# Kernel optimization log

Hardware: AMD Instinct MI355X
Metric: run time of the kernel (lower is better)

Reference implementation:

```python
import jax, jax.numpy as jnp
import numpy as np

N_NODES = 20000
N_EDGES = 200000
N_GRAPHS = 128
IN_DIM = 256
HID = 512
HEADS = 8
C = HID // HEADS  # 64
LAT = 256
NEG_SLOPE = 0.2
BN_EPS = 1e-5


def setup_inputs() -> dict:
    key = jax.random.key(0)
    ks = jax.random.split(key, 24)
    n = lambda k, s, sc=0.05: jax.random.normal(k, s, jnp.float32) * sc
    return {
        'x': jax.random.normal(ks[0], (N_NODES, IN_DIM), jnp.float32),
        'edge_index': jax.random.randint(ks[1], (2, N_EDGES), 0, N_NODES, jnp.int32),
        'batch': jnp.sort(jax.random.randint(ks[2], (N_NODES,), 0, N_GRAPHS, jnp.int32)),
        'Wl0': n(ks[3], (IN_DIM, HID)), 'bl0': n(ks[4], (HID,)),
        'Wr0': n(ks[5], (IN_DIM, HID)), 'br0': n(ks[6], (HID,)),
        'att0': n(ks[7], (HEADS, C)), 'bias0': n(ks[8], (HID,)),
        'Wl1': n(ks[9], (HID, HID)), 'bl1': n(ks[10], (HID,)),
        'Wr1': n(ks[11], (HID, HID)), 'br1': n(ks[12], (HID,)),
        'att1': n(ks[13], (HEADS, C)), 'bias1': n(ks[14], (HID,)),
        'bn_gamma': jnp.ones((HID,), jnp.float32),
        'bn_beta': jnp.zeros((HID,), jnp.float32),
        'bn_mean': n(ks[15], (HID,)),
        'bn_var': jax.random.uniform(ks[16], (HID,), jnp.float32, 0.5, 1.5),
        'Wfc': n(ks[17], (HID, LAT)), 'bfc': n(ks[18], (LAT,)),
    }


def gatv2_layer(x, src, dst, Wl, bl, Wr, br, att, bias):
    # x: [N, F]; returns [N, HEADS*C]. GATv2: e = a . LeakyReLU(Wl x_src + Wr x_dst)
    xl = (x @ Wl + bl).reshape(-1, HEADS, C)  # source transform [N,H,C]
    xr = (x @ Wr + br).reshape(-1, HEADS, C)  # target transform [N,H,C]
    feat = jax.nn.leaky_relu(xl[src] + xr[dst], NEG_SLOPE)     # [E,H,C]
    logits = jnp.einsum('ehc,hc->eh', feat, att)               # [E,H]
    # segment softmax over incoming edges of each target node
    m = jax.ops.segment_max(logits, dst, num_segments=N_NODES)  # [N,H]
    p = jnp.exp(logits - m[dst])
    denom = jax.ops.segment_sum(p, dst, num_segments=N_NODES)   # [N,H]
    alpha = p / (denom[dst] + 1e-16)                            # [E,H]
    msg = xl[src] * alpha[:, :, None]                           # [E,H,C]
    out = jax.ops.segment_sum(msg, dst, num_segments=N_NODES)   # [N,H,C]
    return out.reshape(-1, HEADS * C) + bias


def reference(x, edge_index, batch, Wl0, bl0, Wr0, br0, att0, bias0,
              Wl1, bl1, Wr1, br1, att1, bias1,
              bn_gamma, bn_beta, bn_mean, bn_var, Wfc, bfc):
    src, dst = edge_index[0], edge_index[1]
    # layer 0 + ELU (dropout is identity in eval mode)
    h = jax.nn.elu(gatv2_layer(x, src, dst, Wl0, bl0, Wr0, br0, att0, bias0))
    # layer 1 + ELU
    h = jax.nn.elu(gatv2_layer(h, src, dst, Wl1, bl1, Wr1, br1, att1, bias1))
    # global add pool over graphs
    g = jax.ops.segment_sum(h, batch, num_segments=N_GRAPHS)  # [G, HID]
    # BatchNorm1d (eval mode: running stats)
    g = (g - bn_mean) * jax.lax.rsqrt(bn_var + BN_EPS) * bn_gamma + bn_beta
    return g @ Wfc + bfc  # [G, LAT]
```

## Files before the change

kernel.cpp:

```cpp
#include <hip/hip_runtime.h>
#include <hip/hip_bf16.h>
#include <cstdint>

#define NN 20000
#define NE 200000
#define NG 128
#define HID 512
#define XLR_W 1024

typedef __attribute__((ext_vector_type(4))) float f32x4;
typedef __attribute__((ext_vector_type(8))) short s16x8;

__device__ __forceinline__ float bf2f(unsigned short u) {
  union { unsigned int i; float f; } v; v.i = ((unsigned int)u) << 16; return v.f;
}
__device__ __forceinline__ unsigned short f2bf(float f) {
  union { float f; unsigned int i; } v; v.f = f;
  unsigned int i = v.i + 0x7FFFu + ((v.i >> 16) & 1u);
  return (unsigned short)(i >> 16);
}
__device__ __forceinline__ float asf(unsigned int u) {
  union { unsigned int i; float f; } v; v.i = u; return v.f;
}

#define GLOAD16(gp, lp)                                                        \
  __builtin_amdgcn_global_load_lds(                                            \
      (const __attribute__((address_space(1))) unsigned int*)(gp),             \
      (__attribute__((address_space(3))) unsigned int*)(lp), 16, 0, 0)

__global__ __launch_bounds__(256) void k_prep(const float* __restrict__ x,
                                              unsigned short* __restrict__ xb,
                                              const float* __restrict__ Wl0, const float* __restrict__ bl0,
                                              const float* __restrict__ Wr0, const float* __restrict__ br0,
                                              unsigned short* __restrict__ wt0, float* __restrict__ bcat0,
                                              const float* __restrict__ Wl1, const float* __restrict__ bl1,
                                              const float* __restrict__ Wr1, const float* __restrict__ br1,
                                              unsigned short* __restrict__ wt1, float* __restrict__ bcat1,
                                              int* __restrict__ deg) {
  int b = blockIdx.x, t = threadIdx.x;
  if (b < 79) {
    int i = b * 256 + t;
    if (i < NN) deg[i] = 0;
  } else if (b < 5079) {
    int i = (b - 79) * 256 + t;
    float4 v = ((const float4*)x)[i];
    ushort4 o;
    o.x = f2bf(v.x); o.y = f2bf(v.y); o.z = f2bf(v.z); o.w = f2bf(v.w);
    ((ushort4*)xb)[i] = o;
  } else if (b < 6103) {
    int id = (b - 5079) * 256 + t;
    int nrow = id >> 8, k = id & 255;
    float v = (nrow < HID) ? Wl0[k * HID + nrow] : Wr0[k * HID + (nrow - HID)];
    wt0[id] = f2bf(v);
    if (id < XLR_W) bcat0[id] = (id < HID) ? bl0[id] : br0[id - HID];
  } else {
    int id = (b - 6103) * 256 + t;
    int nrow = id >> 9, k = id & 511;
    float v = (nrow < HID) ? Wl1[k * HID + nrow] : Wr1[k * HID + (nrow - HID)];
    wt1[id] = f2bf(v);
    if (id < XLR_W) bcat1[id] = (id < HID) ? bl1[id] : br1[id - HID];
  }
}

__global__ void k_hist(const int* __restrict__ dst, int* __restrict__ deg, int E) {
  int i = blockIdx.x * blockDim.x + threadIdx.x;
  if (i < E) atomicAdd(&deg[dst[i]], 1);
}

__global__ __launch_bounds__(1024) void k_scan1(const int* __restrict__ deg,
                                                int* __restrict__ offs,
                                                int* __restrict__ btot, int n) {
  __shared__ int wsum[16];
  int t = threadIdx.x;
  int wid = t >> 6, lane = t & 63;
  int i = blockIdx.x * 1024 + t;
  int v = (i < n) ? deg[i] : 0;
  int s = v;
#pragma unroll
  for (int off = 1; off < 64; off <<= 1) {
    int x = __shfl_up(s, off, 64);
    if (lane >= off) s += x;
  }
  if (lane == 63) wsum[wid] = s;
  __syncthreads();
  if (wid == 0) {
    int ws = (lane < 16) ? wsum[lane] : 0;
#pragma unroll
    for (int off = 1; off < 16; off <<= 1) {
      int x = __shfl_up(ws, off, 64);
      if (lane >= off) ws += x;
    }
    if (lane < 16) wsum[lane] = ws;
  }
  __syncthreads();
  int ex = s - v + (wid ? wsum[wid - 1] : 0);
  if (i < n) offs[i] = ex;
  if (t == 1023) btot[blockIdx.x] = ex + v;
}

__global__ __launch_bounds__(1024) void k_scan3(int* __restrict__ offs,
                                                const int* __restrict__ btot,
                                                int* __restrict__ woff, int n, int nb) {
  __shared__ int sbofs;
  int t = threadIdx.x;
  if (t < 64) {
    int v = (t < nb) ? btot[t] : 0;
    int s = v;
#pragma unroll
    for (int off = 1; off < 64; off <<= 1) {
      int x = __shfl_up(s, off, 64);
      if (t >= off) s += x;
    }
    if (t == (int)blockIdx.x) sbofs = s - v;
    if (blockIdx.x == (unsigned)(nb - 1) && t == nb - 1) offs[n] = s;
  }
  __syncthreads();
  int add = sbofs;
  int i = blockIdx.x * 1024 + t;
  if (i < n) {
    int v = offs[i] + add;
    offs[i] = v;
    woff[i] = v;
  }
}

__global__ void k_scatter(const int* __restrict__ src, const int* __restrict__ dst,
                          int* __restrict__ woff, int* __restrict__ src_s, int E) {
  int i = blockIdx.x * blockDim.x + threadIdx.x;
  if (i < E) {
    int d = dst[i];
    int pos = atomicAdd(&woff[d], 1);
    src_s[pos] = src[i];
  }
}

#define BM 128
#define BN 128
#define PLN 4096

__global__ __launch_bounds__(256) void k_gemm(const unsigned short* __restrict__ A,
                                              const unsigned short* __restrict__ Bt,
                                              const float* __restrict__ bias,
                                              unsigned short* __restrict__ C,
                                              int M, int N, int K, int nby) {
  int L = blockIdx.x;
  int by = (L & 7) | ((L >> 6) << 3);
  int bx = (L >> 3) & 7;
  if (by >= nby) return;
  int m0 = by * BM, n0 = bx * BN;

  __shared__ __align__(16) unsigned short As[2 * PLN];
  __shared__ __align__(16) unsigned short Bs[2 * PLN];
  int t = threadIdx.x;
  int wave = t >> 6, lane = t & 63;
  int wm = (wave >> 1) * 64, wn = (wave & 1) * 64;
  int ml = lane & 15, mq = lane >> 4;
  int lr = lane >> 2;
  int qg = (lane & 3) ^ ((lane >> 3) & 3);
  int lq = qg * 8;

  f32x4 acc[4][4];
#pragma unroll
  for (int i = 0; i < 4; i++)
#pragma unroll
    for (int j = 0; j < 4; j++) acc[i][j] = (f32x4)0.0f;

  const unsigned short* gA[4];
  const unsigned short* gB[4];
  unsigned short* lA[4];
  unsigned short* lB[4];
#pragma unroll
  for (int p = 0; p < 2; p++)
#pragma unroll
    for (int h = 0; h < 2; h++) {
      int idx = p * 2 + h;
      int arow = m0 + wave * 32 + h * 16 + lr; if (arow > M - 1) arow = M - 1;
      gA[idx] = A + (size_t)arow * K + p * 32 + lq;
      gB[idx] = Bt + (size_t)(n0 + wave * 32 + h * 16 + lr) * K + p * 32 + lq;
      lA[idx] = &As[p * PLN + (wave * 32 + h * 16) * 32];
      lB[idx] = &Bs[p * PLN + (wave * 32 + h * 16) * 32];
    }

  int qr = (mq ^ ((ml >> 1) & 3)) * 8;

  int T = K >> 6;
  for (int tt = 0; tt < T; tt++) {
#pragma unroll
    for (int idx = 0; idx < 4; idx++) {
      GLOAD16(gA[idx], lA[idx]);
      GLOAD16(gB[idx], lB[idx]);
      gA[idx] += 64; gB[idx] += 64;
    }
    __syncthreads();
#pragma unroll
    for (int kq = 0; kq < 2; kq++) {
      s16x8 af[4], bfr[4];
#pragma unroll
      for (int i = 0; i < 4; i++)
        af[i] = *(const s16x8*)(&As[kq * PLN + (wm + i * 16 + ml) * 32 + qr]);
#pragma unroll
      for (int j = 0; j < 4; j++)
        bfr[j] = *(const s16x8*)(&Bs[kq * PLN + (wn + j * 16 + ml) * 32 + qr]);
#pragma unroll
      for (int i = 0; i < 4; i++)
#pragma unroll
        for (int j = 0; j < 4; j++)
          acc[i][j] = __builtin_amdgcn_mfma_f32_16x16x32_bf16(af[i], bfr[j], acc[i][j], 0, 0, 0);
    }
    __syncthreads();
  }

#pragma unroll
  for (int i = 0; i < 4; i++) {
#pragma unroll
    for (int j = 0; j < 4; j++) {
      int col = n0 + wn + j * 16 + ml;
      float bcol = bias[col];
#pragma unroll
      for (int r = 0; r < 4; r++) {
        int row = m0 + wm + i * 16 + mq * 4 + r;
        if (row < M) C[(size_t)row * N + col] = f2bf(acc[i][j][r] + bcol);
      }
    }
  }
}

__global__ __launch_bounds__(256) void k_attn(const unsigned short* __restrict__ xlr,
                                              const float* __restrict__ att,
                                              const int* __restrict__ offs,
                                              const int* __restrict__ src_s,
                                              const float* __restrict__ bias,
                                              unsigned short* __restrict__ hout) {
  __shared__ float red[4][8][68];
  __shared__ float reds[4][8];
  int n = blockIdx.x;
  int wave = threadIdx.x >> 6, lane = threadIdx.x & 63;
  int h = lane >> 3, k = lane & 7;
  int c = h * 64 + k * 8;
  int s0 = offs[n], s1 = offs[n + 1];

  uint4 uxr = *(const uint4*)(xlr + (size_t)n * XLR_W + HID + c);
  float xr[8];
  xr[0] = asf(uxr.x << 16); xr[1] = asf(uxr.x & 0xFFFF0000u);
  xr[2] = asf(uxr.y << 16); xr[3] = asf(uxr.y & 0xFFFF0000u);
  xr[4] = asf(uxr.z << 16); xr[5] = asf(uxr.z & 0xFFFF0000u);
  xr[6] = asf(uxr.w << 16); xr[7] = asf(uxr.w & 0xFFFF0000u);
  float at[8];
  {
    const float4* ap = (const float4*)(att + c);
    float4 a0 = ap[0], a1 = ap[1];
    at[0] = a0.x; at[1] = a0.y; at[2] = a0.z; at[3] = a0.w;
    at[4] = a1.x; at[5] = a1.y; at[6] = a1.z; at[7] = a1.w;
  }

  float acc[8] = {0.f, 0.f, 0.f, 0.f, 0.f, 0.f, 0.f, 0.f};
  float sum = 0.0f;

  int i = s0 + wave;
  uint4 u_cur = make_uint4(0, 0, 0, 0);
  if (i < s1) {
    int s = src_s[i];
    u_cur = *(const uint4*)(xlr + (size_t)s * XLR_W + c);
  }
  int nx = i + 4;
  for (; i < s1; i += 4) {
    uint4 u = u_cur;
    if (nx < s1) {
      int s = src_s[nx];
      u_cur = *(const uint4*)(xlr + (size_t)s * XLR_W + c);
    }
    nx += 4;

    float xl[8];
    xl[0] = asf(u.x << 16); xl[1] = asf(u.x & 0xFFFF0000u);
    xl[2] = asf(u.y << 16); xl[3] = asf(u.y & 0xFFFF0000u);
    xl[4] = asf(u.z << 16); xl[5] = asf(u.z & 0xFFFF0000u);
    xl[6] = asf(u.w << 16); xl[7] = asf(u.w & 0xFFFF0000u);

    float l = 0.0f;
#pragma unroll
    for (int j = 0; j < 8; j++) {
      float v = xl[j] + xr[j];
      v = fmaf(0.4f, fabsf(v), 0.6f * v);
      l = fmaf(v, at[j], l);
    }
    l += __shfl_xor(l, 1, 64);
    l += __shfl_xor(l, 2, 64);
    l += __shfl_xor(l, 4, 64);

    float p = __expf(l);
    sum += p;
#pragma unroll
    for (int j = 0; j < 8; j++) acc[j] = fmaf(p, xl[j], acc[j]);
  }

#pragma unroll
  for (int j = 0; j < 8; j++) red[wave][h][k * 8 + j] = acc[j];
  if (k == 0) reds[wave][h] = sum;
  __syncthreads();

  int t = threadIdx.x;
  int cc = t * 2;
  int hh = cc >> 6, off = cc & 63;
  float a0 = red[0][hh][off] + red[1][hh][off] + red[2][hh][off] + red[3][hh][off];
  float a1 = red[0][hh][off + 1] + red[1][hh][off + 1] + red[2][hh][off + 1] + red[3][hh][off + 1];
  float sm = reds[0][hh] + reds[1][hh] + reds[2][hh] + reds[3][hh];
  float di = 1.0f / (sm + 1e-16f);
  float o_a = a0 * di + bias[cc];
  float o_b = a1 * di + bias[cc + 1];
  o_a = o_a > 0.0f ? o_a : (__expf(o_a) - 1.0f);
  o_b = o_b > 0.0f ? o_b : (__expf(o_b) - 1.0f);
  unsigned int up = (unsigned int)f2bf(o_a) | ((unsigned int)f2bf(o_b) << 16);
  *(unsigned int*)(hout + (size_t)n * HID + cc) = up;
}

__device__ __forceinline__ int lower_bound(const int* __restrict__ a, int n, int key) {
  int lo = 0, hi = n;
  while (lo < hi) { int mid = (lo + hi) >> 1; if (a[mid] < key) lo = mid + 1; else hi = mid; }
  return lo;
}

__global__ __launch_bounds__(256) void k_pool(const unsigned short* __restrict__ h,
                                              const int* __restrict__ batch,
                                              float* __restrict__ part) {
  int g = blockIdx.x, p = blockIdx.y, t = threadIdx.x;
  int start = lower_bound(batch, NN, g);
  int end = lower_bound(batch, NN, g + 1);
  int cntq = (end - start + 3) >> 2;
  int lo = start + p * cntq;
  int hi = lo + cntq; if (hi > end) hi = end;
  int c = t * 2;
  float a0 = 0.0f, a1 = 0.0f;
  for (int n = lo; n < hi; n++) {
    unsigned int u = *(const unsigned int*)(h + (size_t)n * HID + c);
    a0 += asf(u << 16);
    a1 += asf(u & 0xFFFF0000u);
  }
  float* dstp = part + ((size_t)g * 4 + p) * HID + c;
  dstp[0] = a0;
  dstp[1] = a1;
}

__global__ __launch_bounds__(256) void k_fc(const float* __restrict__ part,
                                            const float* __restrict__ gamma,
                                            const float* __restrict__ beta,
                                            const float* __restrict__ mean,
                                            const float* __restrict__ var,
                                            const float* __restrict__ Wfc,
                                            const float* __restrict__ bfc,
                                            float* __restrict__ out) {
  __shared__ float xsm[512];
  int g = blockIdx.x, t = threadIdx.x;
  for (int c = t; c < HID; c += 256) {
    float s = part[((size_t)g * 4 + 0) * HID + c] + part[((size_t)g * 4 + 1) * HID + c]
            + part[((size_t)g * 4 + 2) * HID + c] + part[((size_t)g * 4 + 3) * HID + c];
    xsm[c] = (s - mean[c]) * rsqrtf(var[c] + 1e-5f) * gamma[c] + beta[c];
  }
  __syncthreads();
  float acc = bfc[t];
#pragma unroll 8
  for (int k = 0; k < 512; k++) acc += xsm[k] * Wfc[k * 256 + t];
  out[g * 256 + t] = acc;
}

extern "C" void kernel_launch(void* const* d_in, const int* in_sizes, int n_in,
                              void* d_out, int out_size, void* d_ws, size_t ws_size,
                              hipStream_t stream) {
  const float* x     = (const float*)d_in[0];
  const int* ei      = (const int*)d_in[1];
  const int* batch   = (const int*)d_in[2];
  const float* Wl0   = (const float*)d_in[3];
  const float* bl0   = (const float*)d_in[4];
  const float* Wr0   = (const float*)d_in[5];
  const float* br0   = (const float*)d_in[6];
  const float* att0  = (const float*)d_in[7];
  const float* bias0 = (const float*)d_in[8];
  const float* Wl1   = (const float*)d_in[9];
  const float* bl1   = (const float*)d_in[10];
  const float* Wr1   = (const float*)d_in[11];
  const float* br1   = (const float*)d_in[12];
  const float* att1  = (const float*)d_in[13];
  const float* bias1 = (const float*)d_in[14];
  const float* gamma = (const float*)d_in[15];
  const float* beta  = (const float*)d_in[16];
  const float* mean  = (const float*)d_in[17];
  const float* var   = (const float*)d_in[18];
  const float* Wfc   = (const float*)d_in[19];
  const float* bfc   = (const float*)d_in[20];

  const int* src = ei;
  const int* dst = ei + NE;

  char* w = (char*)d_ws;
  size_t off = 0;
  auto alloc = [&](size_t bytes) -> void* {
    void* p = w + off;
    off += (bytes + 255) & ~(size_t)255;
    return p;
  };
  int* deg            = (int*)alloc((size_t)NN * 4);
  int* offs           = (int*)alloc((size_t)(NN + 1) * 4);
  int* woff           = (int*)alloc((size_t)NN * 4);
  int* src_s          = (int*)alloc((size_t)NE * 4);
  int* btot           = (int*)alloc((size_t)32 * 4);
  unsigned short* xb  = (unsigned short*)alloc((size_t)NN * 256 * 2);
  unsigned short* xlr = (unsigned short*)alloc((size_t)NN * XLR_W * 2);
  unsigned short* hb  = (unsigned short*)alloc((size_t)NN * HID * 2);
  unsigned short* wt0 = (unsigned short*)alloc((size_t)XLR_W * 256 * 2);
  unsigned short* wt1 = (unsigned short*)alloc((size_t)XLR_W * HID * 2);
  float* bcat0        = (float*)alloc((size_t)XLR_W * 4);
  float* bcat1        = (float*)alloc((size_t)XLR_W * 4);
  float* part         = (float*)alloc((size_t)NG * 4 * HID * 4);

  const int NB = (NN + 1023) / 1024;
  const int NBY = (NN + BM - 1) / BM;
  const int GRID = 64 * ((NBY + 7) / 8);

  k_prep<<<8151, 256, 0, stream>>>(x, xb, Wl0, bl0, Wr0, br0, wt0, bcat0,
                                   Wl1, bl1, Wr1, br1, wt1, bcat1, deg);
  k_hist<<<(NE + 255) / 256, 256, 0, stream>>>(dst, deg, NE);
  k_scan1<<<NB, 1024, 0, stream>>>(deg, offs, btot, NN);
  k_scan3<<<NB, 1024, 0, stream>>>(offs, btot, woff, NN, NB);
  k_scatter<<<(NE + 255) / 256, 256, 0, stream>>>(src, dst, woff, src_s, NE);

  k_gemm<<<GRID, 256, 0, stream>>>(xb, wt0, bcat0, xlr, NN, XLR_W, 256, NBY);
  k_attn<<<NN, 256, 0, stream>>>(xlr, att0, offs, src_s, bias0, hb);

  k_gemm<<<GRID, 256, 0, stream>>>(hb, wt1, bcat1, xlr, NN, XLR_W, 512, NBY);
  k_attn<<<NN, 256, 0, stream>>>(xlr, att1, offs, src_s, bias1, hb);

  k_pool<<<dim3(NG, 4), 256, 0, stream>>>(hb, batch, part);
  k_fc<<<NG, 256, 0, stream>>>(part, gamma, beta, mean, var, Wfc, bfc, (float*)d_out);
}
```

Before: 315.1 us.

## Fuse histogram into first GEMM, single-pass scan, merge pool and FC

Three launches are removed. The degree histogram now runs as extra blocks appended to the first GEMM grid. The two-kernel block scan becomes one kernel that chains block prefixes through a decoupled-lookback status array. Pooling and the FC layer merge into a single kernel with one block per graph. This trades launch overhead and extra passes for a serial spin-wait between scan blocks and less parallelism in pooling (128 blocks instead of 512).

```diff
diff --git a/kernel.cpp b/kernel.cpp
--- a/kernel.cpp
+++ b/kernel.cpp
@@ -36,25 +36,28 @@
                                               const float* __restrict__ Wl1, const float* __restrict__ bl1,
                                               const float* __restrict__ Wr1, const float* __restrict__ br1,
                                               unsigned short* __restrict__ wt1, float* __restrict__ bcat1,
-                                              int* __restrict__ deg) {
+                                              int* __restrict__ deg,
+                                              unsigned long long* __restrict__ st) {
   int b = blockIdx.x, t = threadIdx.x;
   if (b < 79) {
     int i = b * 256 + t;
     if (i < NN) deg[i] = 0;
-  } else if (b < 5079) {
-    int i = (b - 79) * 256 + t;
+  } else if (b == 79) {
+    if (t < 32) st[t] = 0ULL;
+  } else if (b < 5080) {
+    int i = (b - 80) * 256 + t;
     float4 v = ((const float4*)x)[i];
     ushort4 o;
     o.x = f2bf(v.x); o.y = f2bf(v.y); o.z = f2bf(v.z); o.w = f2bf(v.w);
     ((ushort4*)xb)[i] = o;
-  } else if (b < 6103) {
-    int id = (b - 5079) * 256 + t;
+  } else if (b < 6104) {
+    int id = (b - 5080) * 256 + t;
     int nrow = id >> 8, k = id & 255;
     float v = (nrow < HID) ? Wl0[k * HID + nrow] : Wr0[k * HID + (nrow - HID)];
     wt0[id] = f2bf(v);
     if (id < XLR_W) bcat0[id] = (id < HID) ? bl0[id] : br0[id - HID];
   } else {
-    int id = (b - 6103) * 256 + t;
+    int id = (b - 6104) * 256 + t;
     int nrow = id >> 9, k = id & 511;
     float v = (nrow < HID) ? Wl1[k * HID + nrow] : Wr1[k * HID + (nrow - HID)];
     wt1[id] = f2bf(v);
@@ -62,15 +65,13 @@
   }
 }
 
-__global__ void k_hist(const int* __restrict__ dst, int* __restrict__ deg, int E) {
-  int i = blockIdx.x * blockDim.x + threadIdx.x;
-  if (i < E) atomicAdd(&deg[dst[i]], 1);
-}
-
-__global__ __launch_bounds__(1024) void k_scan1(const int* __restrict__ deg,
-                                                int* __restrict__ offs,
-                                                int* __restrict__ btot, int n) {
+__global__ __launch_bounds__(1024) void k_scan(const int* __restrict__ deg,
+                                               int* __restrict__ offs,
+                                               int* __restrict__ woff,
+                                               unsigned long long* __restrict__ st,
+                                               int n) {
   __shared__ int wsum[16];
+  __shared__ int sexcl;
   int t = threadIdx.x;
   int wid = t >> 6, lane = t & 63;
   int i = blockIdx.x * 1024 + t;
@@ -94,33 +95,25 @@
   }
   __syncthreads();
   int ex = s - v + (wid ? wsum[wid - 1] : 0);
-  if (i < n) offs[i] = ex;
-  if (t == 1023) btot[blockIdx.x] = ex + v;
-}
-
-__global__ __launch_bounds__(1024) void k_scan3(int* __restrict__ offs,
-                                                const int* __restrict__ btot,
-                                                int* __restrict__ woff, int n, int nb) {
-  __shared__ int sbofs;
-  int t = threadIdx.x;
-  if (t < 64) {
-    int v = (t < nb) ? btot[t] : 0;
-    int s = v;
-#pragma unroll
-    for (int off = 1; off < 64; off <<= 1) {
-      int x = __shfl_up(s, off, 64);
-      if (t >= off) s += x;
-    }
-    if (t == (int)blockIdx.x) sbofs = s - v;
-    if (blockIdx.x == (unsigned)(nb - 1) && t == nb - 1) offs[n] = s;
+  int bt = wsum[15];
+  if (t == 1023) {
+    int excl = 0;
+    int bid = blockIdx.x;
+    if (bid > 0) {
+      unsigned long long val;
+      do { val = atomicAdd(&st[bid - 1], 0ULL); } while (!(val >> 63));
+      excl = (int)(val & 0xFFFFFFFFULL);
+    }
+    atomicExch(&st[blockIdx.x], (1ULL << 63) | (unsigned long long)(unsigned)(excl + bt));
+    sexcl = excl;
+    if (bid == (int)gridDim.x - 1) offs[n] = excl + bt;
   }
   __syncthreads();
-  int add = sbofs;
-  int i = blockIdx.x * 1024 + t;
+  int base = sexcl;
   if (i < n) {
-    int v = offs[i] + add;
-    offs[i] = v;
-    woff[i] = v;
+    int val = ex + base;
+    offs[i] = val;
+    woff[i] = val;
   }
 }
 
@@ -142,15 +135,23 @@
                                               const unsigned short* __restrict__ Bt,
                                               const float* __restrict__ bias,
                                               unsigned short* __restrict__ C,
-                                              int M, int N, int K, int nby) {
+                                              int M, int N, int K, int nby,
+                                              const int* __restrict__ hdst,
+                                              int* __restrict__ deg,
+                                              int gemmBlocks, int histN) {
+  __shared__ __align__(16) unsigned short As[2 * PLN];
+  __shared__ __align__(16) unsigned short Bs[2 * PLN];
   int L = blockIdx.x;
+  if (L >= gemmBlocks) {
+    int i = (L - gemmBlocks) * 256 + threadIdx.x;
+    if (i < histN) atomicAdd(&deg[hdst[i]], 1);
+    return;
+  }
   int by = (L & 7) | ((L >> 6) << 3);
   int bx = (L >> 3) & 7;
   if (by >= nby) return;
   int m0 = by * BM, n0 = bx * BN;
 
-  __shared__ __align__(16) unsigned short As[2 * PLN];
-  __shared__ __align__(16) unsigned short Bs[2 * PLN];
   int t = threadIdx.x;
   int wave = t >> 6, lane = t & 63;
   int wm = (wave >> 1) * 64, wn = (wave & 1) * 64;
@@ -320,42 +321,28 @@
   return lo;
 }
 
-__global__ __launch_bounds__(256) void k_pool(const unsigned short* __restrict__ h,
-                                              const int* __restrict__ batch,
-                                              float* __restrict__ part) {
-  int g = blockIdx.x, p = blockIdx.y, t = threadIdx.x;
+__global__ __launch_bounds__(256) void k_poolfc(const unsigned short* __restrict__ h,
+                                                const int* __restrict__ batch,
+                                                const float* __restrict__ gamma,
+                                                const float* __restrict__ beta,
+                                                const float* __restrict__ mean,
+                                                const float* __restrict__ var,
+                                                const float* __restrict__ Wfc,
+                                                const float* __restrict__ bfc,
+                                                float* __restrict__ out) {
+  __shared__ float xsm[512];
+  int g = blockIdx.x, t = threadIdx.x;
   int start = lower_bound(batch, NN, g);
   int end = lower_bound(batch, NN, g + 1);
-  int cntq = (end - start + 3) >> 2;
-  int lo = start + p * cntq;
-  int hi = lo + cntq; if (hi > end) hi = end;
   int c = t * 2;
   float a0 = 0.0f, a1 = 0.0f;
-  for (int n = lo; n < hi; n++) {
+  for (int n = start; n < end; n++) {
     unsigned int u = *(const unsigned int*)(h + (size_t)n * HID + c);
     a0 += asf(u << 16);
     a1 += asf(u & 0xFFFF0000u);
   }
-  float* dstp = part + ((size_t)g * 4 + p) * HID + c;
-  dstp[0] = a0;
-  dstp[1] = a1;
-}
-
-__global__ __launch_bounds__(256) void k_fc(const float* __restrict__ part,
-                                            const float* __restrict__ gamma,
-                                            const float* __restrict__ beta,
-                                            const float* __restrict__ mean,
-                                            const float* __restrict__ var,
-                                            const float* __restrict__ Wfc,
-                                            const float* __restrict__ bfc,
-                                            float* __restrict__ out) {
-  __shared__ float xsm[512];
-  int g = blockIdx.x, t = threadIdx.x;
-  for (int c = t; c < HID; c += 256) {
-    float s = part[((size_t)g * 4 + 0) * HID + c] + part[((size_t)g * 4 + 1) * HID + c]
-            + part[((size_t)g * 4 + 2) * HID + c] + part[((size_t)g * 4 + 3) * HID + c];
-    xsm[c] = (s - mean[c]) * rsqrtf(var[c] + 1e-5f) * gamma[c] + beta[c];
-  }
+  xsm[c]     = (a0 - mean[c]) * rsqrtf(var[c] + 1e-5f) * gamma[c] + beta[c];
+  xsm[c + 1] = (a1 - mean[c + 1]) * rsqrtf(var[c + 1] + 1e-5f) * gamma[c + 1] + beta[c + 1];
   __syncthreads();
   float acc = bfc[t];
 #pragma unroll 8
@@ -398,37 +385,33 @@
     off += (bytes + 255) & ~(size_t)255;
     return p;
   };
-  int* deg            = (int*)alloc((size_t)NN * 4);
-  int* offs           = (int*)alloc((size_t)(NN + 1) * 4);
-  int* woff           = (int*)alloc((size_t)NN * 4);
-  int* src_s          = (int*)alloc((size_t)NE * 4);
-  int* btot           = (int*)alloc((size_t)32 * 4);
-  unsigned short* xb  = (unsigned short*)alloc((size_t)NN * 256 * 2);
-  unsigned short* xlr = (unsigned short*)alloc((size_t)NN * XLR_W * 2);
-  unsigned short* hb  = (unsigned short*)alloc((size_t)NN * HID * 2);
-  unsigned short* wt0 = (unsigned short*)alloc((size_t)XLR_W * 256 * 2);
-  unsigned short* wt1 = (unsigned short*)alloc((size_t)XLR_W * HID * 2);
-  float* bcat0        = (float*)alloc((size_t)XLR_W * 4);
-  float* bcat1        = (float*)alloc((size_t)XLR_W * 4);
-  float* part         = (float*)alloc((size_t)NG * 4 * HID * 4);
-
-  const int NB = (NN + 1023) / 1024;
-  const int NBY = (NN + BM - 1) / BM;
+  int* deg                 = (int*)alloc((size_t)NN * 4);
+  int* offs                = (int*)alloc((size_t)(NN + 1) * 4);
+  int* woff                = (int*)alloc((size_t)NN * 4);
+  int* src_s               = (int*)alloc((size_t)NE * 4);
+  unsigned long long* st   = (unsigned long long*)alloc((size_t)32 * 8);
+  unsigned short* xb       = (unsigned short*)alloc((size_t)NN * 256 * 2);
+  unsigned short* xlr      = (unsigned short*)alloc((size_t)NN * XLR_W * 2);
+  unsigned short* hb       = (unsigned short*)alloc((size_t)NN * HID * 2);
+  unsigned short* wt0      = (unsigned short*)alloc((size_t)XLR_W * 256 * 2);
+  unsigned short* wt1      = (unsigned short*)alloc((size_t)XLR_W * HID * 2);
+  float* bcat0             = (float*)alloc((size_t)XLR_W * 4);
+  float* bcat1             = (float*)alloc((size_t)XLR_W * 4);
+
+  const int NB   = (NN + 1023) / 1024;
+  const int NBY  = (NN + BM - 1) / BM;
   const int GRID = 64 * ((NBY + 7) / 8);
-
-  k_prep<<<8151, 256, 0, stream>>>(x, xb, Wl0, bl0, Wr0, br0, wt0, bcat0,
-                                   Wl1, bl1, Wr1, br1, wt1, bcat1, deg);
-  k_hist<<<(NE + 255) / 256, 256, 0, stream>>>(dst, deg, NE);
-  k_scan1<<<NB, 1024, 0, stream>>>(deg, offs, btot, NN);
-  k_scan3<<<NB, 1024, 0, stream>>>(offs, btot, woff, NN, NB);
-  k_scatter<<<(NE + 255) / 256, 256, 0, stream>>>(src, dst, woff, src_s, NE);
-
-  k_gemm<<<GRID, 256, 0, stream>>>(xb, wt0, bcat0, xlr, NN, XLR_W, 256, NBY);
+  const int HB   = (NE + 255) / 256;
+
+  k_prep<<<8152, 256, 0, stream>>>(x, xb, Wl0, bl0, Wr0, br0, wt0, bcat0,
+                                   Wl1, bl1, Wr1, br1, wt1, bcat1, deg, st);
+  k_gemm<<<GRID + HB, 256, 0, stream>>>(xb, wt0, bcat0, xlr, NN, XLR_W, 256, NBY,
+                                        dst, deg, GRID, NE);
+  k_scan<<<NB, 1024, 0, stream>>>(deg, offs, woff, st, NN);
+  k_scatter<<<HB, 256, 0, stream>>>(src, dst, woff, src_s, NE);
   k_attn<<<NN, 256, 0, stream>>>(xlr, att0, offs, src_s, bias0, hb);
-
-  k_gemm<<<GRID, 256, 0, stream>>>(hb, wt1, bcat1, xlr, NN, XLR_W, 512, NBY);
+  k_gemm<<<GRID, 256, 0, stream>>>(hb, wt1, bcat1, xlr, NN, XLR_W, 512, NBY,
+                                   nullptr, nullptr, GRID, 0);
   k_attn<<<NN, 256, 0, stream>>>(xlr, att1, offs, src_s, bias1, hb);
-
-  k_pool<<<dim3(NG, 4), 256, 0, stream>>>(hb, batch, part);
-  k_fc<<<NG, 256, 0, stream>>>(part, gamma, beta, mean, var, Wfc, bfc, (float*)d_out);
-}
+  k_poolfc<<<NG, 256, 0, stream>>>(hb, batch, gamma, beta, mean, var, Wfc, bfc, (float*)d_out);
+}
```

After: 340.8 us. 1.08x slower.
